# Performance work log

Hardware: AMD Instinct MI355X
Metric: run time of the kernel (lower is better)

The kernel has to match this reference:

```python
import jax, jax.numpy as jnp
import numpy as np

B, L, D, NH, NP = 8, 4096, 384, 8, 4


def setup_inputs() -> dict:
    key = jax.random.key(0)
    ks = jax.random.split(key, 16)
    s = 1.0 / np.sqrt(D)
    f32 = jnp.float32
    inp = {
        'query': jax.random.normal(ks[0], (B, L, D), f32),
        'key':   jax.random.normal(ks[1], (B, L, D), f32),
        'value': jax.random.normal(ks[2], (B, L, D), f32),
        # linear weights stored as [in, out]; x @ W + b
        'Wq': jax.random.normal(ks[3], (D, D), f32) * s,
        'bq': jnp.zeros((D,), f32),
        'Wk': jax.random.normal(ks[4], (D, D), f32) * s,
        'bk': jnp.zeros((D,), f32),
        'Wv': jax.random.normal(ks[5], (D, D), f32) * s,
        'bv': jnp.zeros((D,), f32),
        'Woff': jax.random.normal(ks[6], (D, NH * NP * 2), f32) * s,
        'boff': jnp.zeros((NH * NP * 2,), f32),
        'Wwt': jax.random.normal(ks[7], (D, NH * NP), f32) * s,
        'bwt': jnp.zeros((NH * NP,), f32),
        'Wo': jax.random.normal(ks[8], (D, D), f32) * s,
        'bo': jnp.zeros((D,), f32),
        'num_heads': NH,
        'n_points': NP,
    }
    return inp


def reference(query, key, value, Wq, bq, Wk, bk, Wv, bv, Woff, boff, Wwt, bwt, Wo, bo, num_heads, n_points):
    Bq, Lq, Dm = query.shape
    Lk = key.shape[1]
    Lv = value.shape[1]
    hd = Dm // num_heads
    h = w = int(round(np.sqrt(Lk)))  # original: feature_size = int(sqrt(Lk))

    q = query @ Wq + bq          # computed as in original (only its reshape is used via output path)
    k = key @ Wk + bk            # faithful: k_proj is computed but unused downstream
    v = value @ Wv + bv

    # offsets [B, nH, Lq, nP, 2] and softmax point weights [B, nH, Lq, nP]
    off = (query @ Woff + boff).reshape(Bq, Lq, num_heads, n_points, 2).transpose(0, 2, 1, 3, 4)
    wt = jax.nn.softmax((query @ Wwt + bwt).reshape(Bq, Lq, num_heads, n_points).transpose(0, 2, 1, 3), axis=-1)

    # reference grid: ref[...,0] = x (tiled over rows), ref[...,1] = y (repeated over cols)
    yy = jnp.linspace(0.0, 1.0, h)
    xx = jnp.linspace(0.0, 1.0, w)
    gy, gx = jnp.meshgrid(yy, xx, indexing='ij')
    ref = jnp.stack([gx.reshape(-1), gy.reshape(-1)], axis=-1)  # [L, 2]

    loc = jnp.clip(ref[None, None, :, None, :] + off, 0.0, 1.0)  # [B,nH,Lq,nP,2]
    # NOTE: faithful to source, which multiplies component 0 by (h-1) (its 'h' coord)
    ph = loc[..., 0] * (h - 1)   # row pixel coord, in [0, h-1]
    pw = loc[..., 1] * (w - 1)   # col pixel coord, in [0, w-1]

    y0 = jnp.floor(ph)
    x0 = jnp.floor(pw)
    wy = (ph - y0)[..., None]
    wx = (pw - x0)[..., None]
    y0i = y0.astype(jnp.int32)
    x0i = x0.astype(jnp.int32)
    y1i = jnp.minimum(y0i + 1, h - 1)
    x1i = jnp.minimum(x0i + 1, w - 1)

    vh = v.reshape(Bq, Lv, num_heads, hd).transpose(0, 2, 1, 3)  # [B,nH,Lv,hd]

    def gather(yi, xi):
        idx = (yi * w + xi).reshape(Bq, num_heads, Lq * n_points, 1)
        return jnp.take_along_axis(vh, idx, axis=2).reshape(Bq, num_heads, Lq, n_points, hd)

    # bilinear sample (align_corners=True; coords in-range so zero-padding never triggers)
    sampled = ((1 - wy) * ((1 - wx) * gather(y0i, x0i) + wx * gather(y0i, x1i))
               + wy * ((1 - wx) * gather(y1i, x0i) + wx * gather(y1i, x1i)))

    out = jnp.einsum('bhlp,bhlpd->bhld', wt, sampled)  # weighted point aggregation
    out = out.transpose(0, 2, 1, 3).reshape(Bq, Lq, Dm)
    return out @ Wo + bo  # dropout is identity in eval mode
```

## Files before the change

### kernel.cpp

```cpp
#include <hip/hip_runtime.h>
#include <hip/hip_bf16.h>
#include <stdint.h>

using bf16 = __hip_bfloat16;

typedef __attribute__((ext_vector_type(8))) short short8;
typedef __attribute__((ext_vector_type(4))) float float4v;

namespace {
constexpr int kL  = 4096;
constexpr int kD  = 384;
constexpr int kHD = 48;
constexpr int kGW = 64;
constexpr int kM  = 32768;

constexpr size_t nValue = (size_t)kM * kD;
constexpr size_t nW     = (size_t)kD * kD;
constexpr size_t nWcat  = (size_t)96 * kD;

constexpr size_t oWvt  = 0;
constexpr size_t oWot  = oWvt  + nW * 2;
constexpr size_t oWch  = oWot  + nW * 2;
constexpr size_t oWcl  = oWch  + nWcat * 2;
constexpr size_t oBcat = oWcl  + nWcat * 2;
constexpr size_t oVB   = (oBcat + 96 * 4 + 255) & ~size_t(255);
constexpr size_t oProj = oVB   + nValue * 2;
constexpr size_t oAgg  = oProj + (size_t)kM * 96 * 4;
}

__device__ __forceinline__ void load_lds_16(const void* g, void* l) {
  __builtin_amdgcn_global_load_lds((const __attribute__((address_space(1))) void*)g,
                                   (__attribute__((address_space(3))) void*)l,
                                   16, 0, 0);
}

__device__ __forceinline__ short bf16bits(float f) {
  bf16 h = __float2bfloat16(f);
  return *reinterpret_cast<short*>(&h);
}

__device__ __forceinline__ float bf16raw2f(unsigned short u) {
  union { unsigned int i; float f; } c;
  c.i = ((unsigned int)u) << 16;
  return c.f;
}

__global__ void prep_kernel(const float* __restrict__ Wv,
                            const float* __restrict__ Wo,
                            const float* __restrict__ Woff,
                            const float* __restrict__ Wwt,
                            const float* __restrict__ boff,
                            const float* __restrict__ bwt,
                            bf16* __restrict__ Wvt, bf16* __restrict__ Wot,
                            bf16* __restrict__ Wch, bf16* __restrict__ Wcl,
                            float* __restrict__ bcat)
{
  size_t i = (size_t)blockIdx.x * 256 + threadIdx.x;
  if (i < nW) {
    const int n = (int)(i / kD), k = (int)(i % kD);
    Wvt[i] = __float2bfloat16(Wv[(size_t)k * kD + n]);
    return;
  }
  i -= nW;
  if (i < nW) {
    const int n = (int)(i / kD), k = (int)(i % kD);
    Wot[i] = __float2bfloat16(Wo[(size_t)k * kD + n]);
    return;
  }
  i -= nW;
  if (i < nWcat) {
    const int n = (int)(i / kD), k = (int)(i % kD);
    const float val = (n < 64) ? Woff[(size_t)k * 64 + n] : Wwt[(size_t)k * 32 + (n - 64)];
    const bf16 h = __float2bfloat16(val);
    Wch[i] = h;
    Wcl[i] = __float2bfloat16(val - __bfloat162float(h));
    return;
  }
  i -= nWcat;
  if (i < 96) bcat[i] = (i < 64) ? boff[i] : bwt[i - 64];
}

template<bool A_F32, bool OUT_BF16>
__device__ __forceinline__
void mfma_gemm_body(char* smem, int bid,
                    const void* __restrict__ A, const bf16* __restrict__ Bt,
                    const float* __restrict__ bias, void* __restrict__ Cout)
{
  bf16* sA = (bf16*)smem;
  bf16* sB = (bf16*)(smem + 8192);
  const int tid  = threadIdx.x;
  const int lane = tid & 63;
  const int wave = tid >> 6;
  const int bm = bid / 3, bn = bid % 3;
  const int m0 = bm * 128, n0 = bn * 128;
  const int wm = (wave >> 1) * 64, wn = (wave & 1) * 64;
  const int r16 = lane & 15, quad = lane >> 4;

  float4v acc[4][4];
  #pragma unroll
  for (int i = 0; i < 4; ++i)
    #pragma unroll
    for (int j = 0; j < 4; ++j) acc[i][j] = (float4v){0.f, 0.f, 0.f, 0.f};

  const int c0 = tid, c1 = tid + 256;

  for (int kt = 0; kt < 12; ++kt) {
    const int k0 = kt * 32;
    if (A_F32) {
      const float* Af = (const float*)A;
      #pragma unroll
      for (int r = 0; r < 2; ++r) {
        const int e = tid + r * 256;
        const int row = e >> 2, c = e & 3;
        const float* src = Af + (size_t)(m0 + row) * kD + k0 + c * 8;
        const float4 f0 = *(const float4*)src;
        const float4 f1 = *(const float4*)(src + 4);
        short8 hx;
        hx[0] = bf16bits(f0.x); hx[1] = bf16bits(f0.y);
        hx[2] = bf16bits(f0.z); hx[3] = bf16bits(f0.w);
        hx[4] = bf16bits(f1.x); hx[5] = bf16bits(f1.y);
        hx[6] = bf16bits(f1.z); hx[7] = bf16bits(f1.w);
        *(short8*)((char*)sA + e * 16) = hx;
      }
    } else {
      const bf16* Ab = (const bf16*)A;
      load_lds_16(Ab + (size_t)(m0 + (c0 >> 2)) * kD + k0 + (c0 & 3) * 8, (char*)sA + c0 * 16);
      load_lds_16(Ab + (size_t)(m0 + (c1 >> 2)) * kD + k0 + (c1 & 3) * 8, (char*)sA + c1 * 16);
    }
    load_lds_16(Bt + (size_t)(n0 + (c0 >> 2)) * kD + k0 + (c0 & 3) * 8, (char*)sB + c0 * 16);
    load_lds_16(Bt + (size_t)(n0 + (c1 >> 2)) * kD + k0 + (c1 & 3) * 8, (char*)sB + c1 * 16);
    __syncthreads();

    short8 av[4], bv[4];
    #pragma unroll
    for (int i = 0; i < 4; ++i)
      av[i] = *(const short8*)(sA + (wm + i * 16 + r16) * 32 + quad * 8);
    #pragma unroll
    for (int j = 0; j < 4; ++j)
      bv[j] = *(const short8*)(sB + (wn + j * 16 + r16) * 32 + quad * 8);
    #pragma unroll
    for (int i = 0; i < 4; ++i)
      #pragma unroll
      for (int j = 0; j < 4; ++j)
        acc[i][j] = __builtin_amdgcn_mfma_f32_16x16x32_bf16(av[i], bv[j], acc[i][j], 0, 0, 0);
    __syncthreads();
  }

  #pragma unroll
  for (int j = 0; j < 4; ++j) {
    const int col = n0 + wn + j * 16 + r16;
    const float bj = bias[col];
    #pragma unroll
    for (int i = 0; i < 4; ++i) {
      const int mbase = m0 + wm + i * 16 + quad * 4;
      #pragma unroll
      for (int r = 0; r < 4; ++r) {
        const float val = acc[i][j][r] + bj;
        if (OUT_BF16)
          ((bf16*)Cout)[(size_t)(mbase + r) * kD + col] = __float2bfloat16(val);
        else
          ((float*)Cout)[(size_t)(mbase + r) * kD + col] = val;
      }
    }
  }
}

__device__ __forceinline__
void proj_mfma_body(char* smem, int bid,
                    const float* __restrict__ Q,
                    const bf16* __restrict__ WhT, const bf16* __restrict__ WlT,
                    const float* __restrict__ bc, float* __restrict__ proj)
{
  bf16* sAh = (bf16*)smem;
  bf16* sAl = (bf16*)(smem + 8192);
  bf16* sBh = (bf16*)(smem + 16384);
  bf16* sBl = (bf16*)(smem + 22528);
  const int tid  = threadIdx.x;
  const int lane = tid & 63;
  const int wave = tid >> 6;
  const int m0 = bid * 128;
  const int wm = (wave >> 1) * 64, wn = (wave & 1) * 48;
  const int r16 = lane & 15, quad = lane >> 4;

  float4v acc[4][3];
  #pragma unroll
  for (int i = 0; i < 4; ++i)
    #pragma unroll
    for (int j = 0; j < 3; ++j) acc[i][j] = (float4v){0.f, 0.f, 0.f, 0.f};

  for (int kt = 0; kt < 12; ++kt) {
    const int k0 = kt * 32;
    #pragma unroll
    for (int r = 0; r < 2; ++r) {
      const int e = tid + r * 256;
      const int row = e >> 2, c = e & 3;
      const float* src = Q + (size_t)(m0 + row) * kD + k0 + c * 8;
      const float4 f0 = *(const float4*)src;
      const float4 f1 = *(const float4*)(src + 4);
      const float fv[8] = {f0.x, f0.y, f0.z, f0.w, f1.x, f1.y, f1.z, f1.w};
      short8 hx, lx;
      #pragma unroll
      for (int q = 0; q < 8; ++q) {
        const bf16 h = __float2bfloat16(fv[q]);
        hx[q] = *reinterpret_cast<const short*>(&h);
        const bf16 lo = __float2bfloat16(fv[q] - __bfloat162float(h));
        lx[q] = *reinterpret_cast<const short*>(&lo);
      }
      *(short8*)((char*)sAh + e * 16) = hx;
      *(short8*)((char*)sAl + e * 16) = lx;
    }
    {
      int c = tid;
      load_lds_16(WhT + (size_t)(c >> 2) * kD + k0 + (c & 3) * 8, (char*)sBh + c * 16);
      c = tid + 256;
      if (c < 384) {
        load_lds_16(WhT + (size_t)(c >> 2) * kD + k0 + (c & 3) * 8, (char*)sBh + c * 16);
      } else {
        const int cc = c - 384;
        load_lds_16(WlT + (size_t)(cc >> 2) * kD + k0 + (cc & 3) * 8, (char*)sBl + cc * 16);
      }
      const int cc = tid + 128;
      load_lds_16(WlT + (size_t)(cc >> 2) * kD + k0 + (cc & 3) * 8, (char*)sBl + cc * 16);
    }
    __syncthreads();

    short8 avh[4], avl[4];
    #pragma unroll
    for (int i = 0; i < 4; ++i) {
      avh[i] = *(const short8*)(sAh + (wm + i * 16 + r16) * 32 + quad * 8);
      avl[i] = *(const short8*)(sAl + (wm + i * 16 + r16) * 32 + quad * 8);
    }
    #pragma unroll
    for (int j = 0; j < 3; ++j) {
      const short8 bvh = *(const short8*)(sBh + (wn + j * 16 + r16) * 32 + quad * 8);
      const short8 bvl = *(const short8*)(sBl + (wn + j * 16 + r16) * 32 + quad * 8);
      #pragma unroll
      for (int i = 0; i < 4; ++i) {
        acc[i][j] = __builtin_amdgcn_mfma_f32_16x16x32_bf16(avh[i], bvh, acc[i][j], 0, 0, 0);
        acc[i][j] = __builtin_amdgcn_mfma_f32_16x16x32_bf16(avh[i], bvl, acc[i][j], 0, 0, 0);
        acc[i][j] = __builtin_amdgcn_mfma_f32_16x16x32_bf16(avl[i], bvh, acc[i][j], 0, 0, 0);
      }
    }
    __syncthreads();
  }

  #pragma unroll
  for (int j = 0; j < 3; ++j) {
    const int col = wn + j * 16 + r16;
    const float bj = bc[col];
    #pragma unroll
    for (int i = 0; i < 4; ++i) {
      const int mbase = m0 + wm + i * 16 + quad * 4;
      #pragma unroll
      for (int r = 0; r < 4; ++r)
        proj[(size_t)(mbase + r) * 96 + col] = acc[i][j][r] + bj;
    }
  }
}

__global__ __launch_bounds__(256)
void fat_kernel(const float* __restrict__ value, const bf16* __restrict__ Wvt,
                const float* __restrict__ bv,    bf16* __restrict__ vB,
                const float* __restrict__ Q,     const bf16* __restrict__ Wch,
                const bf16* __restrict__ Wcl,    const float* __restrict__ bcat,
                float* __restrict__ proj)
{
  __shared__ __align__(16) char smem[28672];
  const int pb = blockIdx.x;
  if (pb < 256) {
    proj_mfma_body(smem, pb, Q, Wch, Wcl, bcat, proj);
  } else {
    mfma_gemm_body<true, true>(smem, pb - 256, value, Wvt, bv, vB);
  }
}

__global__ __launch_bounds__(256)
void out_gemm_kernel(const bf16* __restrict__ A, const bf16* __restrict__ Bt,
                     const float* __restrict__ bias, float* __restrict__ Cout)
{
  __shared__ __align__(16) char smem[16384];
  mfma_gemm_body<false, false>(smem, blockIdx.x, A, Bt, bias, Cout);
}

__global__ __launch_bounds__(256)
void sample_kernel(const float* __restrict__ proj, const bf16* __restrict__ v,
                   bf16* __restrict__ agg)
{
  const int b   = blockIdx.x & 7;
  const int idx = blockIdx.x >> 3;
  const int t = threadIdx.x;

  __shared__ float sp[2][96];
  __shared__ int4  soff[2][32];
  __shared__ float4 sbw[2][32];
  __shared__ float swt[2][32];

  if (t < 192) {
    const int tok = t / 96, j = t % 96;
    const int token = b * kL + idx * 2 + tok;
    sp[tok][j] = proj[(size_t)token * 96 + j];
  }
  __syncthreads();

  if (t < 64) {
    const int tok = t >> 5, i = t & 31;
    const int l = idx * 2 + tok;
    const float offx = sp[tok][2 * i];
    const float offy = sp[tok][2 * i + 1];
    const float refx = (float)(l % kGW) * (1.0f / 63.0f);
    const float refy = (float)(l / kGW) * (1.0f / 63.0f);
    const float locx = fminf(fmaxf(refx + offx, 0.f), 1.f);
    const float locy = fminf(fmaxf(refy + offy, 0.f), 1.f);
    const float ph = locx * 63.0f;
    const float pw = locy * 63.0f;
    const float fy = floorf(ph), fx = floorf(pw);
    const int y0 = (int)fy, x0 = (int)fx;
    const int y1 = min(y0 + 1, 63), x1 = min(x0 + 1, 63);
    const float wy = ph - fy, wx = pw - fx;
    soff[tok][i] = make_int4((y0 * kGW + x0) * kD, (y0 * kGW + x1) * kD,
                             (y1 * kGW + x0) * kD, (y1 * kGW + x1) * kD);
    sbw[tok][i] = make_float4((1.f - wy) * (1.f - wx), (1.f - wy) * wx,
                              wy * (1.f - wx),         wy * wx);
  } else if (t < 80) {
    const int u = t - 64, tok = u >> 3, hh = u & 7;
    const float* lg = &sp[tok][64 + hh * 4];
    const float m = fmaxf(fmaxf(lg[0], lg[1]), fmaxf(lg[2], lg[3]));
    float e[4], sum = 0.f;
    #pragma unroll
    for (int p = 0; p < 4; ++p) { e[p] = expf(lg[p] - m); sum += e[p]; }
    const float inv = 1.0f / sum;
    #pragma unroll
    for (int p = 0; p < 4; ++p) swt[tok][hh * 4 + p] = e[p] * inv;
  }
  __syncthreads();

  if (t < 192) {
    const int tok = t / 96, q = t % 96;
    const int h = q / 12, dg = (q % 12) * 4;
    const int l = idx * 2 + tok;
    const int hd = h * kHD + dg;
    const unsigned short* vb = (const unsigned short*)(v + (size_t)b * kL * kD + hd);
    float4v acc = (float4v){0.f, 0.f, 0.f, 0.f};
    #pragma unroll
    for (int p = 0; p < 4; ++p) {
      const int i = h * 4 + p;
      const int4  o  = soff[tok][i];
      const float4 bw = sbw[tok][i];
      const float wt = swt[tok][i];
      const ushort4 u0 = *(const ushort4*)(vb + o.x);
      const ushort4 u1 = *(const ushort4*)(vb + o.y);
      const ushort4 u2 = *(const ushort4*)(vb + o.z);
      const ushort4 u3 = *(const ushort4*)(vb + o.w);
      float4v s;
      s[0] = bw.x * bf16raw2f(u0.x) + bw.y * bf16raw2f(u1.x)
           + bw.z * bf16raw2f(u2.x) + bw.w * bf16raw2f(u3.x);
      s[1] = bw.x * bf16raw2f(u0.y) + bw.y * bf16raw2f(u1.y)
           + bw.z * bf16raw2f(u2.y) + bw.w * bf16raw2f(u3.y);
      s[2] = bw.x * bf16raw2f(u0.z) + bw.y * bf16raw2f(u1.z)
           + bw.z * bf16raw2f(u2.z) + bw.w * bf16raw2f(u3.z);
      s[3] = bw.x * bf16raw2f(u0.w) + bw.y * bf16raw2f(u1.w)
           + bw.z * bf16raw2f(u2.w) + bw.w * bf16raw2f(u3.w);
      #pragma unroll
      for (int d = 0; d < 4; ++d) acc[d] += wt * s[d];
    }
    ushort4 outu;
    outu.x = (unsigned short)bf16bits(acc[0]);
    outu.y = (unsigned short)bf16bits(acc[1]);
    outu.z = (unsigned short)bf16bits(acc[2]);
    outu.w = (unsigned short)bf16bits(acc[3]);
    const int token = b * kL + l;
    *(ushort4*)((unsigned short*)agg + (size_t)token * kD + hd) = outu;
  }
}

extern "C" void kernel_launch(void* const* d_in, const int* in_sizes, int n_in,
                              void* d_out, int out_size, void* d_ws, size_t ws_size,
                              hipStream_t stream)
{
  const float* query = (const float*)d_in[0];
  const float* value = (const float*)d_in[2];
  const float* Wv    = (const float*)d_in[7];
  const float* bv    = (const float*)d_in[8];
  const float* Woff  = (const float*)d_in[9];
  const float* boff  = (const float*)d_in[10];
  const float* Wwt   = (const float*)d_in[11];
  const float* bwt   = (const float*)d_in[12];
  const float* Wo    = (const float*)d_in[13];
  const float* bo    = (const float*)d_in[14];
  float* out = (float*)d_out;

  char* ws = (char*)d_ws;
  bf16*  Wvt  = (bf16*)(ws + oWvt);
  bf16*  Wot  = (bf16*)(ws + oWot);
  bf16*  Wch  = (bf16*)(ws + oWch);
  bf16*  Wcl  = (bf16*)(ws + oWcl);
  float* bcat = (float*)(ws + oBcat);
  bf16*  vB   = (bf16*)(ws + oVB);
  float* proj = (float*)(ws + oProj);
  bf16*  aggB = (bf16*)(ws + oAgg);

  const size_t prepN = nW + nW + nWcat + 96;
  prep_kernel<<<dim3((unsigned)((prepN + 255) / 256)), 256, 0, stream>>>(
      Wv, Wo, Woff, Wwt, boff, bwt, Wvt, Wot, Wch, Wcl, bcat);

  fat_kernel<<<dim3(256 + 768), 256, 0, stream>>>(
      value, Wvt, bv, vB, query, Wch, Wcl, bcat, proj);

  sample_kernel<<<dim3(kM / 2), 256, 0, stream>>>(proj, vB, aggB);

  out_gemm_kernel<<<dim3((kM / 128) * 3), 256, 0, stream>>>(aggB, Wot, bo, out);
}
```

Measured before the change: 264.5 us.

## Fuse sampling with output GEMM and double-buffer the projection GEMMs

Merges the bilinear sampling kernel and the output projection GEMM into one tail kernel. Each 512-thread block builds a 128-token bf16 aggregate tile in LDS and immediately multiplies it by Wo, so the aggregate tensor never round-trips through global memory. The softmax weight is folded into the bilinear corner weights. The value and offset projection GEMMs now double-buffer their LDS tiles, loading the next k-slice into registers while the current one runs on MFMA, which removes one barrier per iteration. The cost is much larger LDS use (about 146 KB per tail block, 56 KB in the fat kernel), which limits occupancy, and only 256 tail blocks, which may underfill the GPU.

```diff
diff --git a/kernel.cpp b/kernel.cpp
--- a/kernel.cpp
+++ b/kernel.cpp
@@ -10,9 +10,9 @@
 namespace {
 constexpr int kL  = 4096;
 constexpr int kD  = 384;
-constexpr int kHD = 48;
 constexpr int kGW = 64;
 constexpr int kM  = 32768;
+constexpr int kAP = 392;
 
 constexpr size_t nValue = (size_t)kM * kD;
 constexpr size_t nW     = (size_t)kD * kD;
@@ -25,7 +25,6 @@
 constexpr size_t oBcat = oWcl  + nWcat * 2;
 constexpr size_t oVB   = (oBcat + 96 * 4 + 255) & ~size_t(255);
 constexpr size_t oProj = oVB   + nValue * 2;
-constexpr size_t oAgg  = oProj + (size_t)kM * 96 * 4;
 }
 
 __device__ __forceinline__ void load_lds_16(const void* g, void* l) {
@@ -80,14 +79,13 @@
   if (i < 96) bcat[i] = (i < 64) ? boff[i] : bwt[i - 64];
 }
 
-template<bool A_F32, bool OUT_BF16>
 __device__ __forceinline__
-void mfma_gemm_body(char* smem, int bid,
-                    const void* __restrict__ A, const bf16* __restrict__ Bt,
-                    const float* __restrict__ bias, void* __restrict__ Cout)
+void vgemm_body(char* smem, int bid,
+                const float* __restrict__ A, const bf16* __restrict__ Bt,
+                const float* __restrict__ bias, bf16* __restrict__ Cout)
 {
   bf16* sA = (bf16*)smem;
-  bf16* sB = (bf16*)(smem + 8192);
+  bf16* sB = (bf16*)(smem + 16384);
   const int tid  = threadIdx.x;
   const int lane = tid & 63;
   const int wave = tid >> 6;
@@ -103,47 +101,63 @@
     for (int j = 0; j < 4; ++j) acc[i][j] = (float4v){0.f, 0.f, 0.f, 0.f};
 
   const int c0 = tid, c1 = tid + 256;
+  const int rA0 = c0 >> 2, cA0 = c0 & 3;
+  const int rA1 = c1 >> 2, cA1 = c1 & 3;
+
+  float4 f00, f01, f10, f11;
+
+  {
+    const float* s0 = A + (size_t)(m0 + rA0) * kD + cA0 * 8;
+    f00 = *(const float4*)s0; f01 = *(const float4*)(s0 + 4);
+    const float* s1 = A + (size_t)(m0 + rA1) * kD + cA1 * 8;
+    f10 = *(const float4*)s1; f11 = *(const float4*)(s1 + 4);
+    load_lds_16(Bt + (size_t)(n0 + rA0) * kD + cA0 * 8, (char*)sB + c0 * 16);
+    load_lds_16(Bt + (size_t)(n0 + rA1) * kD + cA1 * 8, (char*)sB + c1 * 16);
+    short8 hx;
+    hx[0]=bf16bits(f00.x); hx[1]=bf16bits(f00.y); hx[2]=bf16bits(f00.z); hx[3]=bf16bits(f00.w);
+    hx[4]=bf16bits(f01.x); hx[5]=bf16bits(f01.y); hx[6]=bf16bits(f01.z); hx[7]=bf16bits(f01.w);
+    *(short8*)((char*)sA + c0 * 16) = hx;
+    hx[0]=bf16bits(f10.x); hx[1]=bf16bits(f10.y); hx[2]=bf16bits(f10.z); hx[3]=bf16bits(f10.w);
+    hx[4]=bf16bits(f11.x); hx[5]=bf16bits(f11.y); hx[6]=bf16bits(f11.z); hx[7]=bf16bits(f11.w);
+    *(short8*)((char*)sA + c1 * 16) = hx;
+  }
+  __syncthreads();
 
   for (int kt = 0; kt < 12; ++kt) {
-    const int k0 = kt * 32;
-    if (A_F32) {
-      const float* Af = (const float*)A;
-      #pragma unroll
-      for (int r = 0; r < 2; ++r) {
-        const int e = tid + r * 256;
-        const int row = e >> 2, c = e & 3;
-        const float* src = Af + (size_t)(m0 + row) * kD + k0 + c * 8;
-        const float4 f0 = *(const float4*)src;
-        const float4 f1 = *(const float4*)(src + 4);
-        short8 hx;
-        hx[0] = bf16bits(f0.x); hx[1] = bf16bits(f0.y);
-        hx[2] = bf16bits(f0.z); hx[3] = bf16bits(f0.w);
-        hx[4] = bf16bits(f1.x); hx[5] = bf16bits(f1.y);
-        hx[6] = bf16bits(f1.z); hx[7] = bf16bits(f1.w);
-        *(short8*)((char*)sA + e * 16) = hx;
-      }
-    } else {
-      const bf16* Ab = (const bf16*)A;
-      load_lds_16(Ab + (size_t)(m0 + (c0 >> 2)) * kD + k0 + (c0 & 3) * 8, (char*)sA + c0 * 16);
-      load_lds_16(Ab + (size_t)(m0 + (c1 >> 2)) * kD + k0 + (c1 & 3) * 8, (char*)sA + c1 * 16);
-    }
-    load_lds_16(Bt + (size_t)(n0 + (c0 >> 2)) * kD + k0 + (c0 & 3) * 8, (char*)sB + c0 * 16);
-    load_lds_16(Bt + (size_t)(n0 + (c1 >> 2)) * kD + k0 + (c1 & 3) * 8, (char*)sB + c1 * 16);
-    __syncthreads();
-
+    const int cur = kt & 1, nxt = cur ^ 1;
+    if (kt < 11) {
+      const int k0n = (kt + 1) * 32;
+      const float* s0 = A + (size_t)(m0 + rA0) * kD + k0n + cA0 * 8;
+      f00 = *(const float4*)s0; f01 = *(const float4*)(s0 + 4);
+      const float* s1 = A + (size_t)(m0 + rA1) * kD + k0n + cA1 * 8;
+      f10 = *(const float4*)s1; f11 = *(const float4*)(s1 + 4);
+      load_lds_16(Bt + (size_t)(n0 + rA0) * kD + k0n + cA0 * 8, (char*)sB + nxt * 8192 + c0 * 16);
+      load_lds_16(Bt + (size_t)(n0 + rA1) * kD + k0n + cA1 * 8, (char*)sB + nxt * 8192 + c1 * 16);
+    }
+    const bf16* sAc = (const bf16*)((char*)sA + cur * 8192);
+    const bf16* sBc = (const bf16*)((char*)sB + cur * 8192);
     short8 av[4], bv[4];
     #pragma unroll
     for (int i = 0; i < 4; ++i)
-      av[i] = *(const short8*)(sA + (wm + i * 16 + r16) * 32 + quad * 8);
+      av[i] = *(const short8*)(sAc + (wm + i * 16 + r16) * 32 + quad * 8);
     #pragma unroll
     for (int j = 0; j < 4; ++j)
-      bv[j] = *(const short8*)(sB + (wn + j * 16 + r16) * 32 + quad * 8);
+      bv[j] = *(const short8*)(sBc + (wn + j * 16 + r16) * 32 + quad * 8);
     #pragma unroll
     for (int i = 0; i < 4; ++i)
       #pragma unroll
       for (int j = 0; j < 4; ++j)
         acc[i][j] = __builtin_amdgcn_mfma_f32_16x16x32_bf16(av[i], bv[j], acc[i][j], 0, 0, 0);
-    __syncthreads();
+    if (kt < 11) {
+      short8 hx;
+      hx[0]=bf16bits(f00.x); hx[1]=bf16bits(f00.y); hx[2]=bf16bits(f00.z); hx[3]=bf16bits(f00.w);
+      hx[4]=bf16bits(f01.x); hx[5]=bf16bits(f01.y); hx[6]=bf16bits(f01.z); hx[7]=bf16bits(f01.w);
+      *(short8*)((char*)sA + nxt * 8192 + c0 * 16) = hx;
+      hx[0]=bf16bits(f10.x); hx[1]=bf16bits(f10.y); hx[2]=bf16bits(f10.z); hx[3]=bf16bits(f10.w);
+      hx[4]=bf16bits(f11.x); hx[5]=bf16bits(f11.y); hx[6]=bf16bits(f11.z); hx[7]=bf16bits(f11.w);
+      *(short8*)((char*)sA + nxt * 8192 + c1 * 16) = hx;
+      __syncthreads();
+    }
   }
 
   #pragma unroll
@@ -154,27 +168,22 @@
     for (int i = 0; i < 4; ++i) {
       const int mbase = m0 + wm + i * 16 + quad * 4;
       #pragma unroll
-      for (int r = 0; r < 4; ++r) {
-        const float val = acc[i][j][r] + bj;
-        if (OUT_BF16)
-          ((bf16*)Cout)[(size_t)(mbase + r) * kD + col] = __float2bfloat16(val);
-        else
-          ((float*)Cout)[(size_t)(mbase + r) * kD + col] = val;
-      }
+      for (int r = 0; r < 4; ++r)
+        Cout[(size_t)(mbase + r) * kD + col] = __float2bfloat16(acc[i][j][r] + bj);
     }
   }
 }
 
 __device__ __forceinline__
-void proj_mfma_body(char* smem, int bid,
-                    const float* __restrict__ Q,
-                    const bf16* __restrict__ WhT, const bf16* __restrict__ WlT,
-                    const float* __restrict__ bc, float* __restrict__ proj)
-{
-  bf16* sAh = (bf16*)smem;
-  bf16* sAl = (bf16*)(smem + 8192);
-  bf16* sBh = (bf16*)(smem + 16384);
-  bf16* sBl = (bf16*)(smem + 22528);
+void proj_body(char* smem, int bid,
+               const float* __restrict__ Q,
+               const bf16* __restrict__ WhT, const bf16* __restrict__ WlT,
+               const float* __restrict__ bc, float* __restrict__ proj)
+{
+  bf16* sAh  = (bf16*)smem;
+  bf16* sAl  = (bf16*)(smem + 16384);
+  char* sBhB = smem + 32768;
+  char* sBlB = smem + 45056;
   const int tid  = threadIdx.x;
   const int lane = tid & 63;
   const int wave = tid >> 6;
@@ -188,52 +197,79 @@
     #pragma unroll
     for (int j = 0; j < 3; ++j) acc[i][j] = (float4v){0.f, 0.f, 0.f, 0.f};
 
+  const int c0 = tid, c1 = tid + 256;
+  const int rA0 = c0 >> 2, cA0 = c0 & 3;
+  const int rA1 = c1 >> 2, cA1 = c1 & 3;
+  const int cB1 = tid + 256;
+  const int cB2 = tid + 128;
+
+  float4 f00, f01, f10, f11;
+
+  auto stageB = [&](int k0, int buf) {
+    load_lds_16(WhT + (size_t)(tid >> 2) * kD + k0 + (tid & 3) * 8, sBhB + buf * 6144 + tid * 16);
+    if (cB1 < 384) {
+      load_lds_16(WhT + (size_t)(cB1 >> 2) * kD + k0 + (cB1 & 3) * 8, sBhB + buf * 6144 + cB1 * 16);
+    } else {
+      const int cc = cB1 - 384;
+      load_lds_16(WlT + (size_t)(cc >> 2) * kD + k0 + (cc & 3) * 8, sBlB + buf * 6144 + cc * 16);
+    }
+    load_lds_16(WlT + (size_t)(cB2 >> 2) * kD + k0 + (cB2 & 3) * 8, sBlB + buf * 6144 + cB2 * 16);
+  };
+  auto castA = [&](int buf) {
+    const float fv0[8] = {f00.x, f00.y, f00.z, f00.w, f01.x, f01.y, f01.z, f01.w};
+    const float fv1[8] = {f10.x, f10.y, f10.z, f10.w, f11.x, f11.y, f11.z, f11.w};
+    short8 hx, lx;
+    #pragma unroll
+    for (int q = 0; q < 8; ++q) {
+      const bf16 h = __float2bfloat16(fv0[q]);
+      hx[q] = *reinterpret_cast<const short*>(&h);
+      const bf16 lo = __float2bfloat16(fv0[q] - __bfloat162float(h));
+      lx[q] = *reinterpret_cast<const short*>(&lo);
+    }
+    *(short8*)((char*)sAh + buf * 8192 + c0 * 16) = hx;
+    *(short8*)((char*)sAl + buf * 8192 + c0 * 16) = lx;
+    #pragma unroll
+    for (int q = 0; q < 8; ++q) {
+      const bf16 h = __float2bfloat16(fv1[q]);
+      hx[q] = *reinterpret_cast<const short*>(&h);
+      const bf16 lo = __float2bfloat16(fv1[q] - __bfloat162float(h));
+      lx[q] = *reinterpret_cast<const short*>(&lo);
+    }
+    *(short8*)((char*)sAh + buf * 8192 + c1 * 16) = hx;
+    *(short8*)((char*)sAl + buf * 8192 + c1 * 16) = lx;
+  };
+  auto loadA = [&](int k0) {
+    const float* s0 = Q + (size_t)(m0 + rA0) * kD + k0 + cA0 * 8;
+    f00 = *(const float4*)s0; f01 = *(const float4*)(s0 + 4);
+    const float* s1 = Q + (size_t)(m0 + rA1) * kD + k0 + cA1 * 8;
+    f10 = *(const float4*)s1; f11 = *(const float4*)(s1 + 4);
+  };
+
+  loadA(0);
+  stageB(0, 0);
+  castA(0);
+  __syncthreads();
+
   for (int kt = 0; kt < 12; ++kt) {
-    const int k0 = kt * 32;
-    #pragma unroll
-    for (int r = 0; r < 2; ++r) {
-      const int e = tid + r * 256;
-      const int row = e >> 2, c = e & 3;
-      const float* src = Q + (size_t)(m0 + row) * kD + k0 + c * 8;
-      const float4 f0 = *(const float4*)src;
-      const float4 f1 = *(const float4*)(src + 4);
-      const float fv[8] = {f0.x, f0.y, f0.z, f0.w, f1.x, f1.y, f1.z, f1.w};
-      short8 hx, lx;
-      #pragma unroll
-      for (int q = 0; q < 8; ++q) {
-        const bf16 h = __float2bfloat16(fv[q]);
-        hx[q] = *reinterpret_cast<const short*>(&h);
-        const bf16 lo = __float2bfloat16(fv[q] - __bfloat162float(h));
-        lx[q] = *reinterpret_cast<const short*>(&lo);
-      }
-      *(short8*)((char*)sAh + e * 16) = hx;
-      *(short8*)((char*)sAl + e * 16) = lx;
-    }
-    {
-      int c = tid;
-      load_lds_16(WhT + (size_t)(c >> 2) * kD + k0 + (c & 3) * 8, (char*)sBh + c * 16);
-      c = tid + 256;
-      if (c < 384) {
-        load_lds_16(WhT + (size_t)(c >> 2) * kD + k0 + (c & 3) * 8, (char*)sBh + c * 16);
-      } else {
-        const int cc = c - 384;
-        load_lds_16(WlT + (size_t)(cc >> 2) * kD + k0 + (cc & 3) * 8, (char*)sBl + cc * 16);
-      }
-      const int cc = tid + 128;
-      load_lds_16(WlT + (size_t)(cc >> 2) * kD + k0 + (cc & 3) * 8, (char*)sBl + cc * 16);
-    }
-    __syncthreads();
-
+    const int cur = kt & 1, nxt = cur ^ 1;
+    if (kt < 11) {
+      loadA((kt + 1) * 32);
+      stageB((kt + 1) * 32, nxt);
+    }
+    const bf16* sAhc = (const bf16*)((char*)sAh + cur * 8192);
+    const bf16* sAlc = (const bf16*)((char*)sAl + cur * 8192);
+    const bf16* sBhc = (const bf16*)(sBhB + cur * 6144);
+    const bf16* sBlc = (const bf16*)(sBlB + cur * 6144);
     short8 avh[4], avl[4];
     #pragma unroll
     for (int i = 0; i < 4; ++i) {
-      avh[i] = *(const short8*)(sAh + (wm + i * 16 + r16) * 32 + quad * 8);
-      avl[i] = *(const short8*)(sAl + (wm + i * 16 + r16) * 32 + quad * 8);
+      avh[i] = *(const short8*)(sAhc + (wm + i * 16 + r16) * 32 + quad * 8);
+      avl[i] = *(const short8*)(sAlc + (wm + i * 16 + r16) * 32 + quad * 8);
     }
     #pragma unroll
     for (int j = 0; j < 3; ++j) {
-      const short8 bvh = *(const short8*)(sBh + (wn + j * 16 + r16) * 32 + quad * 8);
-      const short8 bvl = *(const short8*)(sBl + (wn + j * 16 + r16) * 32 + quad * 8);
+      const short8 bvh = *(const short8*)(sBhc + (wn + j * 16 + r16) * 32 + quad * 8);
+      const short8 bvl = *(const short8*)(sBlc + (wn + j * 16 + r16) * 32 + quad * 8);
       #pragma unroll
       for (int i = 0; i < 4; ++i) {
         acc[i][j] = __builtin_amdgcn_mfma_f32_16x16x32_bf16(avh[i], bvh, acc[i][j], 0, 0, 0);
@@ -241,7 +277,10 @@
         acc[i][j] = __builtin_amdgcn_mfma_f32_16x16x32_bf16(avl[i], bvh, acc[i][j], 0, 0, 0);
       }
     }
-    __syncthreads();
+    if (kt < 11) {
+      castA(nxt);
+      __syncthreads();
+    }
   }
 
   #pragma unroll
@@ -265,111 +304,160 @@
                 const bf16* __restrict__ Wcl,    const float* __restrict__ bcat,
                 float* __restrict__ proj)
 {
-  __shared__ __align__(16) char smem[28672];
+  __shared__ __align__(16) char smem[57344];
   const int pb = blockIdx.x;
   if (pb < 256) {
-    proj_mfma_body(smem, pb, Q, Wch, Wcl, bcat, proj);
+    proj_body(smem, pb, Q, Wch, Wcl, bcat, proj);
   } else {
-    mfma_gemm_body<true, true>(smem, pb - 256, value, Wvt, bv, vB);
-  }
-}
-
-__global__ __launch_bounds__(256)
-void out_gemm_kernel(const bf16* __restrict__ A, const bf16* __restrict__ Bt,
-                     const float* __restrict__ bias, float* __restrict__ Cout)
-{
-  __shared__ __align__(16) char smem[16384];
-  mfma_gemm_body<false, false>(smem, blockIdx.x, A, Bt, bias, Cout);
-}
-
-__global__ __launch_bounds__(256)
-void sample_kernel(const float* __restrict__ proj, const bf16* __restrict__ v,
-                   bf16* __restrict__ agg)
-{
-  const int b   = blockIdx.x & 7;
-  const int idx = blockIdx.x >> 3;
-  const int t = threadIdx.x;
-
-  __shared__ float sp[2][96];
-  __shared__ int4  soff[2][32];
-  __shared__ float4 sbw[2][32];
-  __shared__ float swt[2][32];
-
-  if (t < 192) {
-    const int tok = t / 96, j = t % 96;
-    const int token = b * kL + idx * 2 + tok;
-    sp[tok][j] = proj[(size_t)token * 96 + j];
+    vgemm_body(smem, pb - 256, value, Wvt, bv, vB);
+  }
+}
+
+__global__ __launch_bounds__(512)
+void tail_kernel(const float* __restrict__ proj, const bf16* __restrict__ v,
+                 const bf16* __restrict__ Wot, const float* __restrict__ bo,
+                 float* __restrict__ out)
+{
+  __shared__ __align__(16) char smem[149504];
+  bf16* sAgg = (bf16*)smem;
+  char* aux  = smem + 100352;
+  int4*   scoff = (int4*)aux;
+  float4* scw   = (float4*)(aux + 16384);
+  char*   sBB   = aux;
+
+  const int raw   = blockIdx.x;
+  const int chunk = (raw & 7) * 32 + (raw >> 3);
+  const int m0    = chunk * 128;
+  const int b     = m0 >> 12;
+  const int l0    = m0 & 4095;
+  const int t     = threadIdx.x;
+
+  for (int qt = 0; qt < 4; ++qt) {
+    const int tok0 = qt * 32;
+    #pragma unroll
+    for (int it = 0; it < 2; ++it) {
+      const int task = t + it * 512;
+      const int tl   = task >> 5;
+      const int pt   = task & 31;
+      const int tok  = tok0 + tl;
+      const int l    = l0 + tok;
+      const float* pb_ = proj + (size_t)(m0 + tok) * 96;
+      const float2 off = *(const float2*)(pb_ + 2 * pt);
+      const int h = pt >> 2, p = pt & 3;
+      const float4 lg = *(const float4*)(pb_ + 64 + h * 4);
+      const float g[4] = {lg.x, lg.y, lg.z, lg.w};
+      const float mx = fmaxf(fmaxf(g[0], g[1]), fmaxf(g[2], g[3]));
+      float e[4], sum = 0.f;
+      #pragma unroll
+      for (int jj = 0; jj < 4; ++jj) { e[jj] = expf(g[jj] - mx); sum += e[jj]; }
+      const float wt = e[p] / sum;
+      const float refx = (float)(l & 63) * (1.0f / 63.0f);
+      const float refy = (float)(l >> 6) * (1.0f / 63.0f);
+      const float locx = fminf(fmaxf(refx + off.x, 0.f), 1.f);
+      const float locy = fminf(fmaxf(refy + off.y, 0.f), 1.f);
+      const float ph = locx * 63.0f;
+      const float pw = locy * 63.0f;
+      const float fy = floorf(ph), fx = floorf(pw);
+      const int y0 = (int)fy, x0 = (int)fx;
+      const int y1 = min(y0 + 1, 63), x1 = min(x0 + 1, 63);
+      const float wy = ph - fy, wx = pw - fx;
+      scoff[tl * 32 + pt] = make_int4((y0 * kGW + x0) * kD, (y0 * kGW + x1) * kD,
+                                      (y1 * kGW + x0) * kD, (y1 * kGW + x1) * kD);
+      scw[tl * 32 + pt] = make_float4(wt * (1.f - wy) * (1.f - wx), wt * (1.f - wy) * wx,
+                                      wt * wy * (1.f - wx),         wt * wy * wx);
+    }
+    __syncthreads();
+    #pragma unroll
+    for (int it = 0; it < 6; ++it) {
+      const int task = t + it * 512;
+      const int tl = task / 96;
+      const int q  = task - tl * 96;
+      const int h  = q / 12;
+      const int col = q * 4;
+      const unsigned short* vb = (const unsigned short*)(v + (size_t)b * kL * kD + col);
+      float4v acc = (float4v){0.f, 0.f, 0.f, 0.f};
+      #pragma unroll
+      for (int p = 0; p < 4; ++p) {
+        const int4   o = scoff[tl * 32 + h * 4 + p];
+        const float4 w = scw  [tl * 32 + h * 4 + p];
+        const ushort4 u0 = *(const ushort4*)(vb + o.x);
+        const ushort4 u1 = *(const ushort4*)(vb + o.y);
+        const ushort4 u2 = *(const ushort4*)(vb + o.z);
+        const ushort4 u3 = *(const ushort4*)(vb + o.w);
+        acc[0] += w.x * bf16raw2f(u0.x) + w.y * bf16raw2f(u1.x)
+                + w.z * bf16raw2f(u2.x) + w.w * bf16raw2f(u3.x);
+        acc[1] += w.x * bf16raw2f(u0.y) + w.y * bf16raw2f(u1.y)
+                + w.z * bf16raw2f(u2.y) + w.w * bf16raw2f(u3.y);
+        acc[2] += w.x * bf16raw2f(u0.z) + w.y * bf16raw2f(u1.z)
+                + w.z * bf16raw2f(u2.z) + w.w * bf16raw2f(u3.z);
+        acc[3] += w.x * bf16raw2f(u0.w) + w.y * bf16raw2f(u1.w)
+                + w.z * bf16raw2f(u2.w) + w.w * bf16raw2f(u3.w);
+      }
+      ushort4 ou;
+      ou.x = (unsigned short)bf16bits(acc[0]);
+      ou.y = (unsigned short)bf16bits(acc[1]);
+      ou.z = (unsigned short)bf16bits(acc[2]);
+      ou.w = (unsigned short)bf16bits(acc[3]);
+      *(ushort4*)(sAgg + (size_t)(tok0 + tl) * kAP + col) = ou;
+    }
+    __syncthreads();
+  }
+
+  const int lane = t & 63, wave = t >> 6;
+  const int r16 = lane & 15, quad = lane >> 4;
+  const int wm = (wave >> 2) * 64;
+  const int wn = (wave & 3) * 96;
+  float4v acc2[4][6];
+  #pragma unroll
+  for (int i = 0; i < 4; ++i)
+    #pragma unroll
+    for (int j = 0; j < 6; ++j) acc2[i][j] = (float4v){0.f, 0.f, 0.f, 0.f};
+
+  #pragma unroll
+  for (int r = 0; r < 3; ++r) {
+    const int c = t + r * 512;
+    load_lds_16(Wot + (size_t)(c >> 2) * kD + (c & 3) * 8, sBB + c * 16);
   }
   __syncthreads();
 
-  if (t < 64) {
-    const int tok = t >> 5, i = t & 31;
-    const int l = idx * 2 + tok;
-    const float offx = sp[tok][2 * i];
-    const float offy = sp[tok][2 * i + 1];
-    const float refx = (float)(l % kGW) * (1.0f / 63.0f);
-    const float refy = (float)(l / kGW) * (1.0f / 63.0f);
-    const float locx = fminf(fmaxf(refx + offx, 0.f), 1.f);
-    const float locy = fminf(fmaxf(refy + offy, 0.f), 1.f);
-    const float ph = locx * 63.0f;
-    const float pw = locy * 63.0f;
-    const float fy = floorf(ph), fx = floorf(pw);
-    const int y0 = (int)fy, x0 = (int)fx;
-    const int y1 = min(y0 + 1, 63), x1 = min(x0 + 1, 63);
-    const float wy = ph - fy, wx = pw - fx;
-    soff[tok][i] = make_int4((y0 * kGW + x0) * kD, (y0 * kGW + x1) * kD,
-                             (y1 * kGW + x0) * kD, (y1 * kGW + x1) * kD);
-    sbw[tok][i] = make_float4((1.f - wy) * (1.f - wx), (1.f - wy) * wx,
-                              wy * (1.f - wx),         wy * wx);
-  } else if (t < 80) {
-    const int u = t - 64, tok = u >> 3, hh = u & 7;
-    const float* lg = &sp[tok][64 + hh * 4];
-    const float m = fmaxf(fmaxf(lg[0], lg[1]), fmaxf(lg[2], lg[3]));
-    float e[4], sum = 0.f;
-    #pragma unroll
-    for (int p = 0; p < 4; ++p) { e[p] = expf(lg[p] - m); sum += e[p]; }
-    const float inv = 1.0f / sum;
-    #pragma unroll
-    for (int p = 0; p < 4; ++p) swt[tok][hh * 4 + p] = e[p] * inv;
-  }
-  __syncthreads();
-
-  if (t < 192) {
-    const int tok = t / 96, q = t % 96;
-    const int h = q / 12, dg = (q % 12) * 4;
-    const int l = idx * 2 + tok;
-    const int hd = h * kHD + dg;
-    const unsigned short* vb = (const unsigned short*)(v + (size_t)b * kL * kD + hd);
-    float4v acc = (float4v){0.f, 0.f, 0.f, 0.f};
-    #pragma unroll
-    for (int p = 0; p < 4; ++p) {
-      const int i = h * 4 + p;
-      const int4  o  = soff[tok][i];
-      const float4 bw = sbw[tok][i];
-      const float wt = swt[tok][i];
-      const ushort4 u0 = *(const ushort4*)(vb + o.x);
-      const ushort4 u1 = *(const ushort4*)(vb + o.y);
-      const ushort4 u2 = *(const ushort4*)(vb + o.z);
-      const ushort4 u3 = *(const ushort4*)(vb + o.w);
-      float4v s;
-      s[0] = bw.x * bf16raw2f(u0.x) + bw.y * bf16raw2f(u1.x)
-           + bw.z * bf16raw2f(u2.x) + bw.w * bf16raw2f(u3.x);
-      s[1] = bw.x * bf16raw2f(u0.y) + bw.y * bf16raw2f(u1.y)
-           + bw.z * bf16raw2f(u2.y) + bw.w * bf16raw2f(u3.y);
-      s[2] = bw.x * bf16raw2f(u0.z) + bw.y * bf16raw2f(u1.z)
-           + bw.z * bf16raw2f(u2.z) + bw.w * bf16raw2f(u3.z);
-      s[3] = bw.x * bf16raw2f(u0.w) + bw.y * bf16raw2f(u1.w)
-           + bw.z * bf16raw2f(u2.w) + bw.w * bf16raw2f(u3.w);
-      #pragma unroll
-      for (int d = 0; d < 4; ++d) acc[d] += wt * s[d];
-    }
-    ushort4 outu;
-    outu.x = (unsigned short)bf16bits(acc[0]);
-    outu.y = (unsigned short)bf16bits(acc[1]);
-    outu.z = (unsigned short)bf16bits(acc[2]);
-    outu.w = (unsigned short)bf16bits(acc[3]);
-    const int token = b * kL + l;
-    *(ushort4*)((unsigned short*)agg + (size_t)token * kD + hd) = outu;
+  for (int kt = 0; kt < 12; ++kt) {
+    const int cur = kt & 1;
+    if (kt < 11) {
+      const int k0n = (kt + 1) * 32;
+      #pragma unroll
+      for (int r = 0; r < 3; ++r) {
+        const int c = t + r * 512;
+        load_lds_16(Wot + (size_t)(c >> 2) * kD + k0n + (c & 3) * 8,
+                    sBB + (cur ^ 1) * 24576 + c * 16);
+      }
+    }
+    const int k0 = kt * 32;
+    const bf16* sBc = (const bf16*)(sBB + cur * 24576);
+    short8 av[4];
+    #pragma unroll
+    for (int i = 0; i < 4; ++i)
+      av[i] = *(const short8*)(sAgg + (size_t)(wm + i * 16 + r16) * kAP + k0 + quad * 8);
+    #pragma unroll
+    for (int j = 0; j < 6; ++j) {
+      const short8 bvj = *(const short8*)(sBc + (wn + j * 16 + r16) * 32 + quad * 8);
+      #pragma unroll
+      for (int i = 0; i < 4; ++i)
+        acc2[i][j] = __builtin_amdgcn_mfma_f32_16x16x32_bf16(av[i], bvj, acc2[i][j], 0, 0, 0);
+    }
+    if (kt < 11) __syncthreads();
+  }
+
+  #pragma unroll
+  for (int j = 0; j < 6; ++j) {
+    const int col = wn + j * 16 + r16;
+    const float bj = bo[col];
+    #pragma unroll
+    for (int i = 0; i < 4; ++i) {
+      const int mb = m0 + wm + i * 16 + quad * 4;
+      #pragma unroll
+      for (int r = 0; r < 4; ++r)
+        out[(size_t)(mb + r) * kD + col] = acc2[i][j][r] + bj;
+    }
   }
 }
 
@@ -397,7 +485,6 @@
   float* bcat = (float*)(ws + oBcat);
   bf16*  vB   = (bf16*)(ws + oVB);
   float* proj = (float*)(ws + oProj);
-  bf16*  aggB = (bf16*)(ws + oAgg);
 
   const size_t prepN = nW + nW + nWcat + 96;
   prep_kernel<<<dim3((unsigned)((prepN + 255) / 256)), 256, 0, stream>>>(
@@ -406,7 +493,5 @@
   fat_kernel<<<dim3(256 + 768), 256, 0, stream>>>(
       value, Wvt, bv, vB, query, Wch, Wcl, bcat, proj);
 
-  sample_kernel<<<dim3(kM / 2), 256, 0, stream>>>(proj, vB, aggB);
-
-  out_gemm_kernel<<<dim3((kM / 128) * 3), 256, 0, stream>>>(aggB, Wot, bo, out);
-}
+  tail_kernel<<<dim3(256), 512, 0, stream>>>(proj, vB, Wot, bo, out);
+}
```

After: 269.9 us. +2.1%, slower.
